# Optimization experiments

Hardware: AMD Instinct MI355X
Metric: run time of the kernel (lower is better)

Reference implementation:

```python
import jax, jax.numpy as jnp
import numpy as np

B, N, E = 32, 116, 1346
IN_V, IN_E, H, OUT = 116, 5, 64, 4
NEG_SLOPE = 0.01  # torch LeakyReLU default


def setup_inputs() -> dict:
    key = jax.random.key(0)
    ks = jax.random.split(key, 13)
    return {
        "H_v": jax.random.normal(ks[0], (B * N, IN_V), jnp.float32),
        "H_e": jax.random.normal(ks[1], (B * E, IN_E), jnp.float32),
        "adj_v": jax.random.uniform(ks[2], (B * N, N), jnp.float32),
        "adj_e": jax.random.uniform(ks[3], (B * E, E), jnp.float32),
        "T": jax.random.uniform(ks[4], (B * N, E), jnp.float32),
        "W_v": jax.random.normal(ks[5], (IN_V, H), jnp.float32) * (1.0 / np.sqrt(H)),
        "p_v": jax.random.normal(ks[6], (1, IN_E), jnp.float32),
        "b_v": jax.random.normal(ks[7], (H,), jnp.float32) * 0.01,
        "W_e": jax.random.normal(ks[8], (IN_E, H), jnp.float32) * (1.0 / np.sqrt(H)),
        "p_e": jax.random.normal(ks[9], (1, H), jnp.float32),
        "b_e": jax.random.normal(ks[10], (H,), jnp.float32) * 0.01,
        "W_fc": jax.random.normal(ks[11], (H, OUT), jnp.float32) * (1.0 / np.sqrt(OUT)),
        "b_fc": jax.random.normal(ks[12], (OUT,), jnp.float32) * 0.01,
    }


def _net(H_v, H_e, adj_v, adj_e, T, W_v, p_v, b_v, W_e, p_e, b_e, W_fc, b_fc):
    # reshape flat [B*N, ...] / [B*E, ...] layouts to batched, as in AlternateConvolution.forward
    Hv = H_v.reshape(B, N, IN_V)
    He = H_e.reshape(B, E, IN_E)
    Av = adj_v.reshape(B, N, N)
    Ae = adj_e.reshape(B, E, E)
    Tm = T.reshape(B, N, E)
    eyeN = jnp.eye(N, dtype=bool)
    eyeE = jnp.eye(E, dtype=bool)

    # ---- node layer (AlternateConvolution, node_layer=True) ----
    de = jnp.einsum('bef,f->be', He, p_v[0])                      # H_e @ p^T -> diag values [B,E]
    mult1 = jnp.einsum('bne,be,bme->bnm', Tm, de, Tm)             # T diag(de) T^T
    M1 = jnp.where(eyeN, 1.0, mult1)                              # ones on diagonal
    adjA = M1 * Av
    Hv = jnp.einsum('bnm,bmh->bnh', adjA, Hv @ W_v) + b_v         # [B,N,H]
    Hv = jax.nn.leaky_relu(Hv, NEG_SLOPE)

    # ---- edge layer (AlternateConvolution, node_layer=False) ----
    dv = jnp.einsum('bnh,h->bn', Hv, p_e[0])                      # H_v @ p^T -> diag values [B,N]
    mult2 = jnp.einsum('bne,bn,bnf->bef', Tm, dv, Tm)             # T^T diag(dv) T
    M3 = jnp.where(eyeE, 1.0, mult2)
    adjE = M3 * Ae
    adjE = adjE / (jnp.max(adjE, axis=2, keepdims=True) + 1e-10)  # row-max normalize
    He = jnp.einsum('bef,bfh->beh', adjE, He @ W_e) + b_e         # [B,E,H]
    He = jax.nn.leaky_relu(He, NEG_SLOPE)

    # ---- mean graph pooling over nodes + classifier head (dropout off in eval) ----
    pooled = Hv.mean(axis=1)                                      # [B,H]
    return pooled @ W_fc + b_fc                                   # [B,OUT]


def reference(H_v, H_e, adj_v, adj_e, T, W_v, p_v, b_v, W_e, p_e, b_e, W_fc, b_fc):
    return _net(H_v, H_e, adj_v, adj_e, T, W_v, p_v, b_v, W_e, p_e, b_e, W_fc, b_fc)
```

## Files before the change

kernel.cpp:

```cpp
#include <hip/hip_runtime.h>

#define BATCH 32
#define NN 116
#define EE 1346
#define HH 64
#define SPLITS 8
#define ECH 170
#define MBLK 256
#define HVBLK 116
#define GRID1 (MBLK + HVBLK + 1)

typedef __attribute__((ext_vector_type(8))) short bf16x8;
typedef __attribute__((ext_vector_type(4))) float f32x4;

__device__ __forceinline__ unsigned int pack_bf16(float a, float b) {
    union { float f; unsigned int u; } ua, ub;
    ua.f = a; ub.f = b;
    unsigned int lo = (ua.u + 0x7FFFu + ((ua.u >> 16) & 1u)) >> 16;
    unsigned int hi = (ub.u + 0x7FFFu + ((ub.u >> 16) & 1u)) >> 16;
    return lo | (hi << 16);
}
__device__ __forceinline__ unsigned short bf16_1(float a) {
    union { float f; unsigned int u; } ua; ua.f = a;
    return (unsigned short)((ua.u + 0x7FFFu + ((ua.u >> 16) & 1u)) >> 16);
}
__device__ __forceinline__ float bf2f(unsigned int bits16) {
    union { unsigned int u; float f; } x; x.u = bits16 << 16;
    return x.f;
}

__global__ __launch_bounds__(512) void stage1_kernel(
    const float* __restrict__ T, const float* __restrict__ He,
    const float* __restrict__ pv,
    const float* __restrict__ Hv, const float* __restrict__ Wv,
    const float* __restrict__ bfc,
    unsigned short* __restrict__ part16, float* __restrict__ HvW,
    float* __restrict__ out)
{
    const int blk = blockIdx.x;
    const int tid = threadIdx.x;

    __shared__ float del[192];
    __shared__ unsigned int Tt[128 * 32];
    __shared__ unsigned int dTt[128 * 32];

    if (blk < MBLK) {
        const int s = blk & 7, b = blk >> 3;
        const int e0 = s * ECH;
        const int cnt = min(ECH, EE - e0);
        const int nsteps = 3;

        {
            const float p0 = pv[0], p1 = pv[1], p2 = pv[2], p3 = pv[3], p4 = pv[4];
            for (int i = tid; i < 192; i += 512) {
                float v = 0.f;
                if (i < cnt) {
                    const float* he = He + (size_t)(b * EE + e0 + i) * 5;
                    v = he[0]*p0 + he[1]*p1 + he[2]*p2 + he[3]*p3 + he[4]*p4;
                }
                del[i] = v;
            }
        }

        const int srow = tid >> 2;
        const int q    = tid & 3;
        const float* Trow = T + ((size_t)b * NN + srow) * EE + e0;

        float2 pf[8];
        auto pref = [&](int c) {
            const int k0 = c * 64 + q * 16;
            #pragma unroll
            for (int j = 0; j < 8; ++j) {
                float2 v = {0.f, 0.f};
                const int k = k0 + 2 * j;
                if (srow < NN && k + 1 < cnt) v = *(const float2*)&Trow[k];
                else if (srow < NN && k < cnt) v.x = Trow[k];
                pf[j] = v;
            }
        };
        auto wlds = [&](int c) {
            const int k0 = c * 64 + q * 16;
            uint4 t0, t1, d0, d1;
            unsigned int* tp0 = &t0.x;  unsigned int* tp1 = &t1.x;
            unsigned int* dp0 = &d0.x;  unsigned int* dp1 = &d1.x;
            #pragma unroll
            for (int j = 0; j < 4; ++j) {
                const float2 va = pf[j];
                const float2 vb = pf[4 + j];
                const float2 da = *(const float2*)&del[k0 + 2 * j];
                const float2 db = *(const float2*)&del[k0 + 8 + 2 * j];
                tp0[j] = pack_bf16(va.x, va.y);
                tp1[j] = pack_bf16(vb.x, vb.y);
                dp0[j] = pack_bf16(va.x * da.x, va.y * da.y);
                dp1[j] = pack_bf16(vb.x * db.x, vb.y * db.y);
            }
            const int swz = (srow & 7) << 4;
            const int bo  = srow * 128 + q * 32;
            *(uint4*)((char*)Tt  + ((bo) ^ swz))      = t0;
            *(uint4*)((char*)Tt  + ((bo + 16) ^ swz)) = t1;
            *(uint4*)((char*)dTt + ((bo) ^ swz))      = d0;
            *(uint4*)((char*)dTt + ((bo + 16) ^ swz)) = d1;
        };

        const int w = tid >> 6, lane = tid & 63;
        const int wr = w >> 2, wc = w & 3;
        const int rl = lane & 15, g = lane >> 4;

        auto fragT = [&](const unsigned int* base, int row, int kkb) -> bf16x8 {
            return *(const bf16x8*)((const char*)base + ((row * 128 + kkb + g * 16) ^ ((row & 7) << 4)));
        };

        f32x4 acc[4][2] = {};

        pref(0);
        __syncthreads();

        for (int c = 0; c < nsteps; ++c) {
            wlds(c);
            __syncthreads();
            if (c + 1 < nsteps) pref(c + 1);
            #pragma unroll
            for (int kk = 0; kk < 2; ++kk) {
                bf16x8 af[4], bf[2];
                #pragma unroll
                for (int i = 0; i < 4; ++i) af[i] = fragT(dTt, wr * 64 + i * 16 + rl, kk * 64);
                #pragma unroll
                for (int j = 0; j < 2; ++j) bf[j] = fragT(Tt,  wc * 32 + j * 16 + rl, kk * 64);
                #pragma unroll
                for (int tn = 0; tn < 4; ++tn)
                    #pragma unroll
                    for (int tm = 0; tm < 2; ++tm)
                        acc[tn][tm] = __builtin_amdgcn_mfma_f32_16x16x32_bf16(
                            af[tn], bf[tm], acc[tn][tm], 0, 0, 0);
            }
            __syncthreads();
        }

        #pragma unroll
        for (int tn = 0; tn < 4; ++tn) {
            #pragma unroll
            for (int r = 0; r < 4; ++r) {
                const int grow = wr * 64 + tn * 16 + g * 4 + r;
                if (grow >= NN) continue;
                unsigned short* rowp = part16 + (((size_t)b * NN + grow) * SPLITS + s) * 128;
                #pragma unroll
                for (int tm = 0; tm < 2; ++tm)
                    rowp[wc * 32 + tm * 16 + rl] = bf16_1(acc[tn][tm][r]);
            }
        }
    } else if (blk < MBLK + HVBLK) {
        const int l0 = (blk - MBLK) * 32 + (tid >> 6) * 4;
        const int h  = tid & 63;
        const float* hv0 = Hv + (size_t)(l0 + 0) * NN;
        const float* hv1 = Hv + (size_t)(l0 + 1) * NN;
        const float* hv2 = Hv + (size_t)(l0 + 2) * NN;
        const float* hv3 = Hv + (size_t)(l0 + 3) * NN;
        float a0 = 0.f, a1 = 0.f, a2 = 0.f, a3 = 0.f;
        #pragma unroll 4
        for (int k = 0; k < NN; ++k) {
            const float wv = Wv[k * HH + h];
            a0 = fmaf(hv0[k], wv, a0);
            a1 = fmaf(hv1[k], wv, a1);
            a2 = fmaf(hv2[k], wv, a2);
            a3 = fmaf(hv3[k], wv, a3);
        }
        HvW[(size_t)(l0 + 0) * HH + h] = a0;
        HvW[(size_t)(l0 + 1) * HH + h] = a1;
        HvW[(size_t)(l0 + 2) * HH + h] = a2;
        HvW[(size_t)(l0 + 3) * HH + h] = a3;
    } else {
        if (tid < BATCH * 4) out[tid] = bfc[tid & 3];
    }
}

__global__ __launch_bounds__(256) void stage2_kernel(
    const unsigned short* __restrict__ part16, const float* __restrict__ Av,
    const float* __restrict__ HvW, const float* __restrict__ bv,
    const float* __restrict__ Wfc, float* __restrict__ out)
{
    const int blk = blockIdx.x;
    const int b = blk >> 3;
    const int n0 = (blk & 7) * 16;
    const int tid = threadIdx.x;
    const int w = tid >> 6, lane = tid & 63;
    const int rl = lane & 15, g = lane >> 4;

    __shared__ unsigned int Cb[4096];
    __shared__ unsigned int Ab[1024];
    __shared__ float sl[64];

    for (int idx = tid; idx < 64 * 64; idx += 256) {
        const int h = idx & 63, np = idx >> 6;
        const int n = 2 * np;
        const float v0 = (n < NN)     ? HvW[((size_t)b * NN + n) * HH + h]     : 0.f;
        const float v1 = (n + 1 < NN) ? HvW[((size_t)b * NN + n + 1) * HH + h] : 0.f;
        *(unsigned int*)((char*)Cb + ((h * 256 + np * 4) ^ ((h & 7) << 4))) = pack_bf16(v0, v1);
    }

    {
        const int r = tid >> 4, m0 = (tid & 15) * 8;
        const int n = n0 + r;
        float ms[8] = {0.f,0.f,0.f,0.f,0.f,0.f,0.f,0.f};
        unsigned int outw[4];
        if (n < NN) {
            const unsigned short* pp = part16 + (((size_t)b * NN + n) * SPLITS) * 128 + m0;
            #pragma unroll
            for (int s = 0; s < SPLITS; ++s) {
                const uint4 u = *(const uint4*)(pp + (size_t)s * 128);
                const unsigned int* up = &u.x;
                #pragma unroll
                for (int j = 0; j < 4; ++j) {
                    ms[2*j]   += bf2f(up[j] & 0xffffu);
                    ms[2*j+1] += bf2f(up[j] >> 16);
                }
            }
            const float* avp = Av + ((size_t)b * NN + n) * NN;
            #pragma unroll
            for (int j = 0; j < 4; ++j) {
                const int m = m0 + 2 * j;
                const float a0 = (m < NN)     ? avp[m]     : 0.f;
                const float a1 = (m + 1 < NN) ? avp[m + 1] : 0.f;
                const float v0 = a0 * ((m     == n) ? 1.0f : ms[2*j]);
                const float v1 = a1 * ((m + 1 == n) ? 1.0f : ms[2*j+1]);
                outw[j] = pack_bf16(v0, v1);
            }
        } else {
            outw[0] = outw[1] = outw[2] = outw[3] = 0u;
        }
        *(uint4*)((char*)Ab + ((r * 256 + m0 * 2) ^ ((r & 7) << 4))) = *(uint4*)outw;
    }
    __syncthreads();

    f32x4 acc = {};
    #pragma unroll
    for (int kk = 0; kk < 4; ++kk) {
        const int hrow = w * 16 + rl;
        const bf16x8 a  = *(const bf16x8*)((const char*)Ab +
                          ((rl * 256 + kk * 64 + g * 16) ^ ((rl & 7) << 4)));
        const bf16x8 bb = *(const bf16x8*)((const char*)Cb +
                          ((hrow * 256 + kk * 64 + g * 16) ^ ((hrow & 7) << 4)));
        acc = __builtin_amdgcn_mfma_f32_16x16x32_bf16(a, bb, acc, 0, 0, 0);
    }
    {
        const int h = w * 16 + rl;
        const float bias = bv[h];
        float s = 0.f;
        #pragma unroll
        for (int r = 0; r < 4; ++r) {
            const int n = n0 + g * 4 + r;
            if (n < NN) {
                const float x = acc[r] + bias;
                s += (x >= 0.f) ? x : 0.01f * x;
            }
        }
        s += __shfl_xor(s, 16);
        s += __shfl_xor(s, 32);
        if (g == 0) sl[h] = s;
    }
    __syncthreads();

    if (tid < 4) {
        float a = 0.f;
        #pragma unroll 16
        for (int k = 0; k < HH; ++k)
            a = fmaf(sl[k], Wfc[k * 4 + tid], a);
        atomicAdd(&out[b * 4 + tid], a * (1.0f / NN));
    }
}

extern "C" void kernel_launch(void* const* d_in, const int* in_sizes, int n_in,
                              void* d_out, int out_size, void* d_ws, size_t ws_size,
                              hipStream_t stream) {
    const float* Hv  = (const float*)d_in[0];
    const float* He  = (const float*)d_in[1];
    const float* Av  = (const float*)d_in[2];
    const float* T_  = (const float*)d_in[4];
    const float* Wv  = (const float*)d_in[5];
    const float* pv  = (const float*)d_in[6];
    const float* bv  = (const float*)d_in[7];
    const float* Wfc = (const float*)d_in[11];
    const float* bfc = (const float*)d_in[12];
    float* out = (float*)d_out;

    unsigned short* part16 = (unsigned short*)d_ws;
    float* HvW = (float*)(part16 + (size_t)BATCH * NN * SPLITS * 128);

    stage1_kernel<<<GRID1, 512, 0, stream>>>(
        T_, He, pv, Hv, Wv, bfc, part16, HvW, out);
    stage2_kernel<<<BATCH * 8, 256, 0, stream>>>(
        part16, Av, HvW, bv, Wfc, out);
}
```

Measured before the change: 32.91 us.

## Fuse both stages into one persistent kernel with a global atomic barrier

Merges the stage1 and stage2 kernels into a single 256-block launch. Blocks are separated by an atomic-counter grid barrier spinning with s_sleep, and the counter is reset by a hipMemsetAsync. The HvW projection work moves from dedicated blocks onto the first 232 blocks, two rows per wave instead of four. This removes one kernel launch and the gap between launches, but adds a memset, a spin barrier, and heavier per-block work. It also relies on all 256 blocks being co-resident, since otherwise the barrier deadlocks.

```diff
diff --git a/kernel.cpp b/kernel.cpp
--- a/kernel.cpp
+++ b/kernel.cpp
@@ -6,9 +6,7 @@
 #define HH 64
 #define SPLITS 8
 #define ECH 170
-#define MBLK 256
-#define HVBLK 116
-#define GRID1 (MBLK + HVBLK + 1)
+#define NBLOCKS 256
 
 typedef __attribute__((ext_vector_type(8))) short bf16x8;
 typedef __attribute__((ext_vector_type(4))) float f32x4;
@@ -29,13 +27,14 @@
     return x.f;
 }
 
-__global__ __launch_bounds__(512) void stage1_kernel(
+__global__ __launch_bounds__(512) void fused_kernel(
     const float* __restrict__ T, const float* __restrict__ He,
     const float* __restrict__ pv,
     const float* __restrict__ Hv, const float* __restrict__ Wv,
-    const float* __restrict__ bfc,
+    const float* __restrict__ bfc, const float* __restrict__ Av,
+    const float* __restrict__ bv, const float* __restrict__ Wfc,
     unsigned short* __restrict__ part16, float* __restrict__ HvW,
-    float* __restrict__ out)
+    unsigned int* __restrict__ ctr, float* __restrict__ out)
 {
     const int blk = blockIdx.x;
     const int tid = threadIdx.x;
@@ -43,8 +42,13 @@
     __shared__ float del[192];
     __shared__ unsigned int Tt[128 * 32];
     __shared__ unsigned int dTt[128 * 32];
-
-    if (blk < MBLK) {
+    __shared__ unsigned int Cb[4096];
+    __shared__ unsigned int Ab[1024];
+    __shared__ float sl[64];
+
+    if (blk == 0 && tid < BATCH * 4) out[tid] = bfc[tid & 3];
+
+    {
         const int s = blk & 7, b = blk >> 3;
         const int e0 = s * ECH;
         const int cnt = min(ECH, EE - e0);
@@ -148,123 +152,116 @@
                     rowp[wc * 32 + tm * 16 + rl] = bf16_1(acc[tn][tm][r]);
             }
         }
-    } else if (blk < MBLK + HVBLK) {
-        const int l0 = (blk - MBLK) * 32 + (tid >> 6) * 4;
-        const int h  = tid & 63;
+    }
+
+    if (blk < 232) {
+        const int w = tid >> 6, h = tid & 63;
+        const int l0 = blk * 16 + w * 2;
         const float* hv0 = Hv + (size_t)(l0 + 0) * NN;
         const float* hv1 = Hv + (size_t)(l0 + 1) * NN;
-        const float* hv2 = Hv + (size_t)(l0 + 2) * NN;
-        const float* hv3 = Hv + (size_t)(l0 + 3) * NN;
-        float a0 = 0.f, a1 = 0.f, a2 = 0.f, a3 = 0.f;
+        float a0 = 0.f, a1 = 0.f;
         #pragma unroll 4
         for (int k = 0; k < NN; ++k) {
             const float wv = Wv[k * HH + h];
             a0 = fmaf(hv0[k], wv, a0);
             a1 = fmaf(hv1[k], wv, a1);
-            a2 = fmaf(hv2[k], wv, a2);
-            a3 = fmaf(hv3[k], wv, a3);
         }
         HvW[(size_t)(l0 + 0) * HH + h] = a0;
         HvW[(size_t)(l0 + 1) * HH + h] = a1;
-        HvW[(size_t)(l0 + 2) * HH + h] = a2;
-        HvW[(size_t)(l0 + 3) * HH + h] = a3;
-    } else {
-        if (tid < BATCH * 4) out[tid] = bfc[tid & 3];
-    }
-}
-
-__global__ __launch_bounds__(256) void stage2_kernel(
-    const unsigned short* __restrict__ part16, const float* __restrict__ Av,
-    const float* __restrict__ HvW, const float* __restrict__ bv,
-    const float* __restrict__ Wfc, float* __restrict__ out)
-{
-    const int blk = blockIdx.x;
-    const int b = blk >> 3;
-    const int n0 = (blk & 7) * 16;
-    const int tid = threadIdx.x;
-    const int w = tid >> 6, lane = tid & 63;
-    const int rl = lane & 15, g = lane >> 4;
-
-    __shared__ unsigned int Cb[4096];
-    __shared__ unsigned int Ab[1024];
-    __shared__ float sl[64];
-
-    for (int idx = tid; idx < 64 * 64; idx += 256) {
-        const int h = idx & 63, np = idx >> 6;
-        const int n = 2 * np;
-        const float v0 = (n < NN)     ? HvW[((size_t)b * NN + n) * HH + h]     : 0.f;
-        const float v1 = (n + 1 < NN) ? HvW[((size_t)b * NN + n + 1) * HH + h] : 0.f;
-        *(unsigned int*)((char*)Cb + ((h * 256 + np * 4) ^ ((h & 7) << 4))) = pack_bf16(v0, v1);
-    }
+    }
+
+    __threadfence();
+    __syncthreads();
+    if (tid == 0) {
+        atomicAdd(ctr, 1u);
+        while (atomicAdd(ctr, 0u) < NBLOCKS) { __builtin_amdgcn_s_sleep(8); }
+    }
+    __syncthreads();
+    __threadfence();
 
     {
-        const int r = tid >> 4, m0 = (tid & 15) * 8;
-        const int n = n0 + r;
-        float ms[8] = {0.f,0.f,0.f,0.f,0.f,0.f,0.f,0.f};
-        unsigned int outw[4];
-        if (n < NN) {
-            const unsigned short* pp = part16 + (((size_t)b * NN + n) * SPLITS) * 128 + m0;
-            #pragma unroll
-            for (int s = 0; s < SPLITS; ++s) {
-                const uint4 u = *(const uint4*)(pp + (size_t)s * 128);
-                const unsigned int* up = &u.x;
+        const int b  = blk >> 3;
+        const int n0 = (blk & 7) * 16;
+        const int w = tid >> 6, lane = tid & 63;
+        const int rl = lane & 15, g = lane >> 4;
+
+        for (int idx = tid; idx < 64 * 64; idx += 512) {
+            const int h = idx & 63, np = idx >> 6;
+            const int n = 2 * np;
+            const float v0 = (n < NN)     ? HvW[((size_t)b * NN + n) * HH + h]     : 0.f;
+            const float v1 = (n + 1 < NN) ? HvW[((size_t)b * NN + n + 1) * HH + h] : 0.f;
+            *(unsigned int*)((char*)Cb + ((h * 256 + np * 4) ^ ((h & 7) << 4))) = pack_bf16(v0, v1);
+        }
+
+        if (tid < 256) {
+            const int r = tid >> 4, m0 = (tid & 15) * 8;
+            const int n = n0 + r;
+            float ms[8] = {0.f,0.f,0.f,0.f,0.f,0.f,0.f,0.f};
+            unsigned int outw[4];
+            if (n < NN) {
+                const unsigned short* pp = part16 + (((size_t)b * NN + n) * SPLITS) * 128 + m0;
+                #pragma unroll
+                for (int s = 0; s < SPLITS; ++s) {
+                    const uint4 u = *(const uint4*)(pp + (size_t)s * 128);
+                    const unsigned int* up = &u.x;
+                    #pragma unroll
+                    for (int j = 0; j < 4; ++j) {
+                        ms[2*j]   += bf2f(up[j] & 0xffffu);
+                        ms[2*j+1] += bf2f(up[j] >> 16);
+                    }
+                }
+                const float* avp = Av + ((size_t)b * NN + n) * NN;
                 #pragma unroll
                 for (int j = 0; j < 4; ++j) {
-                    ms[2*j]   += bf2f(up[j] & 0xffffu);
-                    ms[2*j+1] += bf2f(up[j] >> 16);
-                }
-            }
-            const float* avp = Av + ((size_t)b * NN + n) * NN;
-            #pragma unroll
-            for (int j = 0; j < 4; ++j) {
-                const int m = m0 + 2 * j;
-                const float a0 = (m < NN)     ? avp[m]     : 0.f;
-                const float a1 = (m + 1 < NN) ? avp[m + 1] : 0.f;
-                const float v0 = a0 * ((m     == n) ? 1.0f : ms[2*j]);
-                const float v1 = a1 * ((m + 1 == n) ? 1.0f : ms[2*j+1]);
-                outw[j] = pack_bf16(v0, v1);
-            }
-        } else {
-            outw[0] = outw[1] = outw[2] = outw[3] = 0u;
-        }
-        *(uint4*)((char*)Ab + ((r * 256 + m0 * 2) ^ ((r & 7) << 4))) = *(uint4*)outw;
-    }
-    __syncthreads();
-
-    f32x4 acc = {};
-    #pragma unroll
-    for (int kk = 0; kk < 4; ++kk) {
-        const int hrow = w * 16 + rl;
-        const bf16x8 a  = *(const bf16x8*)((const char*)Ab +
-                          ((rl * 256 + kk * 64 + g * 16) ^ ((rl & 7) << 4)));
-        const bf16x8 bb = *(const bf16x8*)((const char*)Cb +
-                          ((hrow * 256 + kk * 64 + g * 16) ^ ((hrow & 7) << 4)));
-        acc = __builtin_amdgcn_mfma_f32_16x16x32_bf16(a, bb, acc, 0, 0, 0);
-    }
-    {
-        const int h = w * 16 + rl;
-        const float bias = bv[h];
-        float s = 0.f;
-        #pragma unroll
-        for (int r = 0; r < 4; ++r) {
-            const int n = n0 + g * 4 + r;
-            if (n < NN) {
-                const float x = acc[r] + bias;
-                s += (x >= 0.f) ? x : 0.01f * x;
-            }
-        }
-        s += __shfl_xor(s, 16);
-        s += __shfl_xor(s, 32);
-        if (g == 0) sl[h] = s;
-    }
-    __syncthreads();
-
-    if (tid < 4) {
-        float a = 0.f;
-        #pragma unroll 16
-        for (int k = 0; k < HH; ++k)
-            a = fmaf(sl[k], Wfc[k * 4 + tid], a);
-        atomicAdd(&out[b * 4 + tid], a * (1.0f / NN));
+                    const int m = m0 + 2 * j;
+                    const float a0 = (m < NN)     ? avp[m]     : 0.f;
+                    const float a1 = (m + 1 < NN) ? avp[m + 1] : 0.f;
+                    const float v0 = a0 * ((m     == n) ? 1.0f : ms[2*j]);
+                    const float v1 = a1 * ((m + 1 == n) ? 1.0f : ms[2*j+1]);
+                    outw[j] = pack_bf16(v0, v1);
+                }
+            } else {
+                outw[0] = outw[1] = outw[2] = outw[3] = 0u;
+            }
+            *(uint4*)((char*)Ab + ((r * 256 + m0 * 2) ^ ((r & 7) << 4))) = *(uint4*)outw;
+        }
+        __syncthreads();
+
+        if (w < 4) {
+            f32x4 acc = {};
+            #pragma unroll
+            for (int kk = 0; kk < 4; ++kk) {
+                const int hrow = w * 16 + rl;
+                const bf16x8 a  = *(const bf16x8*)((const char*)Ab +
+                                  ((rl * 256 + kk * 64 + g * 16) ^ ((rl & 7) << 4)));
+                const bf16x8 bb = *(const bf16x8*)((const char*)Cb +
+                                  ((hrow * 256 + kk * 64 + g * 16) ^ ((hrow & 7) << 4)));
+                acc = __builtin_amdgcn_mfma_f32_16x16x32_bf16(a, bb, acc, 0, 0, 0);
+            }
+            const int h = w * 16 + rl;
+            const float bias = bv[h];
+            float s = 0.f;
+            #pragma unroll
+            for (int r = 0; r < 4; ++r) {
+                const int n = n0 + g * 4 + r;
+                if (n < NN) {
+                    const float x = acc[r] + bias;
+                    s += (x >= 0.f) ? x : 0.01f * x;
+                }
+            }
+            s += __shfl_xor(s, 16);
+            s += __shfl_xor(s, 32);
+            if (g == 0) sl[h] = s;
+        }
+        __syncthreads();
+
+        if (tid < 4) {
+            float a = 0.f;
+            #pragma unroll 16
+            for (int k = 0; k < HH; ++k)
+                a = fmaf(sl[k], Wfc[k * 4 + tid], a);
+            atomicAdd(&out[b * 4 + tid], a * (1.0f / NN));
+        }
     }
 }
 
@@ -284,9 +281,9 @@
 
     unsigned short* part16 = (unsigned short*)d_ws;
     float* HvW = (float*)(part16 + (size_t)BATCH * NN * SPLITS * 128);
-
-    stage1_kernel<<<GRID1, 512, 0, stream>>>(
-        T_, He, pv, Hv, Wv, bfc, part16, HvW, out);
-    stage2_kernel<<<BATCH * 8, 256, 0, stream>>>(
-        part16, Av, HvW, bv, Wfc, out);
-}
+    unsigned int* ctr = (unsigned int*)(HvW + (size_t)BATCH * NN * HH);
+
+    hipMemsetAsync(ctr, 0, sizeof(unsigned int), stream);
+    fused_kernel<<<NBLOCKS, 512, 0, stream>>>(
+        T_, He, pv, Hv, Wv, bfc, Av, bv, Wfc, part16, HvW, ctr, out);
+}
```

Result: slower. 113.2 us (+243.9%).
